# Performance work log

Measured on AMD Instinct MI355X. Metric: run time of the kernel, lower is better.

The kernel has to match this reference:

```python
import jax, jax.numpy as jnp
import numpy as np

N_NODES = 50000
N_EDGES = 800000
N_GRAPHS = 128
INPUT_DIM = 64
HIDDEN = 64       # num_heads * dim_per_head = 4 * 16
N_HEADS = 4
DK = HIDDEN // N_HEADS   # 16, per-head key/query dim
DV = HIDDEN // N_HEADS   # 16, per-head value dim
NUM_LAYERS = 4           # -> 3 GIN layers
OUT_DIM = 16
LN_EPS = 1e-5


def layer_norm(x, g, b):
    mu = jnp.mean(x, axis=-1, keepdims=True)
    var = jnp.mean(jnp.square(x - mu), axis=-1, keepdims=True)
    return (x - mu) * jax.lax.rsqrt(var + LN_EPS) * g + b


def sab_block(x, Wq, Wk, Wv, Wo, ln_g, ln_b, add_residual):
    # x: [N, S, D_in]; pre-LN self-attention block (Set Transformer SAB)
    xin = layer_norm(x, ln_g, ln_b)
    q = jnp.einsum('nsd,dhk->nshk', xin, Wq)   # [N,S,H,dk]
    k = jnp.einsum('nsd,dhk->nshk', xin, Wk)
    v = jnp.einsum('nsd,dhk->nshk', xin, Wv)   # [N,S,H,dv]
    scores = jnp.einsum('nqhk,nshk->nhqs', q, k) / jnp.sqrt(jnp.asarray(DK, x.dtype))
    att = jax.nn.softmax(scores, axis=-1)
    o = jnp.einsum('nhqs,nshk->nqhk', att, v)
    o = o.reshape(o.shape[0], o.shape[1], N_HEADS * DV)
    o = o @ Wo                                  # [N,S,dim_out]
    if add_residual:
        o = o + x
    return o


def gin_aggregate(h, src, dst):
    # sum-neighbor aggregation; eps=0, learn_eps=False -> (1+0)*h + sum_nbrs
    msg = jax.ops.segment_sum(h[src], dst, num_segments=N_NODES)
    return h + msg


def setup_inputs() -> dict:
    key = jax.random.key(0)
    ks = jax.random.split(key, 16)
    s = 0.05
    feat = jax.random.normal(ks[0], (N_NODES, 4 * INPUT_DIM), dtype=jnp.float32)
    src = jax.random.randint(ks[1], (N_EDGES,), 0, N_NODES)
    dst = jax.random.randint(ks[2], (N_EDGES,), 0, N_NODES)
    graph_ids = jnp.sort(jax.random.randint(ks[3], (N_NODES,), 0, N_GRAPHS))
    L = NUM_LAYERS - 1  # 3 GIN layers, all same shapes (input_dim == hidden)
    Wq = jax.random.normal(ks[4], (L, HIDDEN, N_HEADS, DK), dtype=jnp.float32) * s
    Wk = jax.random.normal(ks[5], (L, HIDDEN, N_HEADS, DK), dtype=jnp.float32) * s
    Wv = jax.random.normal(ks[6], (L, HIDDEN, N_HEADS, DV), dtype=jnp.float32) * s
    Wo = jax.random.normal(ks[7], (L, N_HEADS * DV, HIDDEN), dtype=jnp.float32) * s
    sab_ln_g = jnp.ones((L, HIDDEN), dtype=jnp.float32)
    sab_ln_b = jnp.zeros((L, HIDDEN), dtype=jnp.float32)
    ln1_g = jnp.ones((L, HIDDEN), dtype=jnp.float32)
    ln1_b = jnp.zeros((L, HIDDEN), dtype=jnp.float32)
    ln2_g = jnp.ones((L, HIDDEN), dtype=jnp.float32)
    ln2_b = jnp.zeros((L, HIDDEN), dtype=jnp.float32)
    W_pred = jax.random.normal(ks[8], (NUM_LAYERS, HIDDEN, OUT_DIM), dtype=jnp.float32) * s
    b_pred = jnp.zeros((NUM_LAYERS, OUT_DIM), dtype=jnp.float32)
    return {"feat": feat, "src": src, "dst": dst, "graph_ids": graph_ids,
            "Wq": Wq, "Wk": Wk, "Wv": Wv, "Wo": Wo,
            "sab_ln_g": sab_ln_g, "sab_ln_b": sab_ln_b,
            "ln1_g": ln1_g, "ln1_b": ln1_b, "ln2_g": ln2_g, "ln2_b": ln2_b,
            "W_pred": W_pred, "b_pred": b_pred}


def reference(feat, src, dst, graph_ids, Wq, Wk, Wv, Wo,
              sab_ln_g, sab_ln_b, ln1_g, ln1_b, ln2_g, ln2_b, W_pred, b_pred):
    h = feat.reshape(N_NODES, -1, INPUT_DIM)   # [N, S, D]
    hidden_rep = [h]
    for i in range(NUM_LAYERS - 1):
        if i == 0:
            agg = gin_aggregate(h, src, dst)
            h = sab_block(agg, Wq[i], Wk[i], Wv[i], Wo[i],
                          sab_ln_g[i], sab_ln_b[i], add_residual=False)
        else:
            h_pre = layer_norm(h, ln1_g[i], ln1_b[i])
            agg = gin_aggregate(h_pre, src, dst)
            h = h + sab_block(agg, Wq[i], Wk[i], Wv[i], Wo[i],
                              sab_ln_g[i], sab_ln_b[i], add_residual=True)
        hidden_rep.append(layer_norm(jax.nn.relu(h), ln2_g[i], ln2_b[i]))
    score = jnp.zeros((N_GRAPHS, hidden_rep[0].shape[1], OUT_DIM), dtype=feat.dtype)
    for i, hh in enumerate(hidden_rep):
        pooled = jax.ops.segment_sum(hh, graph_ids, num_segments=N_GRAPHS)  # [B,S,D]
        score = score + pooled @ W_pred[i] + b_pred[i]
    return score
```

## Files before the change

kernel.cpp:

```cpp
#include <hip/hip_runtime.h>

#define NN 50000
#define NE 800000
#define NG 128
#define RREP 16
#define RSTRIDE 50048

typedef __attribute__((ext_vector_type(8))) short short8;
typedef __attribute__((ext_vector_type(4))) float f32x4;

__device__ __forceinline__ unsigned short f2bf(float f){
  union { float f; unsigned int u; } v; v.f = f;
  return (unsigned short)((v.u + 0x7fffu + ((v.u >> 16) & 1u)) >> 16);
}
__device__ __forceinline__ float bf2f(unsigned short h){
  union { unsigned int u; float f; } v; v.u = ((unsigned int)h) << 16;
  return v.f;
}

__global__ __launch_bounds__(256) void k_goff(const int* __restrict__ gid,
                                              int* __restrict__ goff){
  int i = blockIdx.x*256 + threadIdx.x;
  if (i >= NN) return;
  int c = gid[i];
  int p = (i == 0) ? -1 : gid[i-1];
  for (int g = p+1; g <= c; ++g) goff[g] = i;
  if (i == NN-1){
    for (int g = c+1; g <= NG; ++g) goff[g] = NN;
  }
}

__global__ __launch_bounds__(256) void k_count_rep(const int* __restrict__ idx,
                                                   int* __restrict__ cnt_rep, int n){
  int i = blockIdx.x*256 + threadIdx.x;
  int r = blockIdx.x & (RREP-1);
  if (i < n) atomicAdd(&cnt_rep[r*RSTRIDE + idx[i]], 1);
}

__global__ __launch_bounds__(256) void k_reduce_rep(const int* __restrict__ cnt_rep,
                                                    int* __restrict__ cnt){
  int i = blockIdx.x*256 + threadIdx.x;
  if (i < NN){
    int s = 0;
    #pragma unroll
    for (int r=0; r<RREP; ++r) s += cnt_rep[r*RSTRIDE + i];
    cnt[i] = s;
  }
}

__global__ __launch_bounds__(256) void k_blocksum(const int* __restrict__ in, int n,
                                                  int* __restrict__ bsum){
  __shared__ int ws4[4];
  int i = blockIdx.x*256 + threadIdx.x;
  int v = (i < n) ? in[i] : 0;
  #pragma unroll
  for (int d=1; d<64; d<<=1) v += __shfl_xor(v, d);
  int lane = threadIdx.x & 63, w = threadIdx.x >> 6;
  if (lane == 0) ws4[w] = v;
  __syncthreads();
  if (threadIdx.x == 0) bsum[blockIdx.x] = ws4[0]+ws4[1]+ws4[2]+ws4[3];
}

__global__ __launch_bounds__(256) void k_scan_small(const int* __restrict__ in, int n,
                                                    int* __restrict__ out){
  __shared__ int wsum[4];
  int tid = threadIdx.x, lane = tid & 63, w = tid >> 6;
  int v = (tid < n) ? in[tid] : 0;
  int x = v;
  #pragma unroll
  for (int d=1; d<64; d<<=1){ int y = __shfl_up(x, d); if (lane >= d) x += y; }
  if (lane == 63) wsum[w] = x;
  __syncthreads();
  int pre2 = 0;
  for (int j=0; j<w; ++j) pre2 += wsum[j];
  int incl = x + pre2;
  if (tid < n) out[tid] = incl - v;
  if (tid == n-1) out[n] = incl;
}

__global__ __launch_bounds__(256) void k_scan_apply(const int* __restrict__ in, int n,
                                                    const int* __restrict__ boff,
                                                    int* __restrict__ out){
  __shared__ int wsum[4];
  int tid = threadIdx.x, lane = tid & 63, w = tid >> 6;
  int i = blockIdx.x*256 + tid;
  int v = (i < n) ? in[i] : 0;
  int x = v;
  #pragma unroll
  for (int d=1; d<64; d<<=1){ int y = __shfl_up(x, d); if (lane >= d) x += y; }
  if (lane == 63) wsum[w] = x;
  __syncthreads();
  int pre2 = boff[blockIdx.x];
  for (int j=0; j<w; ++j) pre2 += wsum[j];
  int excl = x - v + pre2;
  if (i < n){
    out[i] = excl;
    if (i == n-1) out[n] = excl + v;
  }
}

__global__ __launch_bounds__(256) void k_fpos_rep(const int* __restrict__ cnt_rep,
                                                  const int* __restrict__ off,
                                                  int* __restrict__ fpos_rep){
  int i = blockIdx.x*256 + threadIdx.x;
  if (i < NN){
    int p = off[i];
    #pragma unroll
    for (int r=0; r<RREP; ++r){
      fpos_rep[r*RSTRIDE + i] = p;
      p += cnt_rep[r*RSTRIDE + i];
    }
  }
}

__global__ __launch_bounds__(256) void k_fill_rep(const int* __restrict__ src,
                                                  const int* __restrict__ dst,
                                                  int* __restrict__ fpos_rep,
                                                  int* __restrict__ csr, int n){
  int i = blockIdx.x*256 + threadIdx.x;
  int r = blockIdx.x & (RREP-1);
  if (i < n){
    int p = atomicAdd(&fpos_rep[r*RSTRIDE + dst[i]], 1);
    csr[p] = src[i];
  }
}

__global__ __launch_bounds__(256) void k_wt(const float* __restrict__ Wq,
                                            const float* __restrict__ Wk,
                                            const float* __restrict__ Wv,
                                            const float* __restrict__ Wo,
                                            unsigned short* __restrict__ Wt){
  int gid = blockIdx.x*256 + threadIdx.x;
  int l   = gid >> 14;
  int rem = gid & 16383;
  int mat = rem >> 12;
  int idx = rem & 4095;
  int c = idx >> 6, n = idx & 63;
  const float* srcp = (mat==0)?Wq:(mat==1)?Wk:(mat==2)?Wv:Wo;
  float v = srcp[l*4096 + idx];
  Wt[l*16384 + (mat*64 + n)*64 + c] = f2bf(v);
}

__global__ __launch_bounds__(256) void k_f2bf(const float* __restrict__ in,
                                              unsigned short* __restrict__ out){
  int i = blockIdx.x*256 + threadIdx.x;
  float4 v = ((const float4*)in)[i];
  ushort4 o; o.x=f2bf(v.x); o.y=f2bf(v.y); o.z=f2bf(v.z); o.w=f2bf(v.w);
  ((ushort4*)out)[i] = o;
}

__global__ __launch_bounds__(256) void k_aggregate(const unsigned short* __restrict__ pre,
                                                   const int* __restrict__ off,
                                                   const int* __restrict__ csr,
                                                   float* __restrict__ agg){
  int w = threadIdx.x >> 6, lane = threadIdx.x & 63;
  int node = blockIdx.x*4 + w;
  int s = off[node], e = off[node+1];
  const ushort4* base = (const ushort4*)pre;
  ushort4 u = base[node*64 + lane];
  float a0 = bf2f(u.x), a1 = bf2f(u.y), a2 = bf2f(u.z), a3 = bf2f(u.w);
  int i = s;
  for (; i + 4 <= e; i += 4){
    int n0 = csr[i], n1 = csr[i+1], n2 = csr[i+2], n3 = csr[i+3];
    ushort4 u0 = base[n0*64 + lane], u1 = base[n1*64 + lane];
    ushort4 u2 = base[n2*64 + lane], u3 = base[n3*64 + lane];
    a0 += bf2f(u0.x)+bf2f(u1.x)+bf2f(u2.x)+bf2f(u3.x);
    a1 += bf2f(u0.y)+bf2f(u1.y)+bf2f(u2.y)+bf2f(u3.y);
    a2 += bf2f(u0.z)+bf2f(u1.z)+bf2f(u2.z)+bf2f(u3.z);
    a3 += bf2f(u0.w)+bf2f(u1.w)+bf2f(u2.w)+bf2f(u3.w);
  }
  for (; i < e; ++i){
    int n0 = csr[i];
    ushort4 u0 = base[n0*64 + lane];
    a0 += bf2f(u0.x); a1 += bf2f(u0.y); a2 += bf2f(u0.z); a3 += bf2f(u0.w);
  }
  ((float4*)agg)[node*64 + lane] = make_float4(a0, a1, a2, a3);
}

__global__ __launch_bounds__(256) void k_sab(float* __restrict__ agg,
                                             float* __restrict__ h,
                                             unsigned short* __restrict__ pre_next,
                                             const unsigned short* __restrict__ Wt,
                                             const float* __restrict__ lng,
                                             const float* __restrict__ lnb,
                                             const float* __restrict__ g2,
                                             const float* __restrict__ b2,
                                             const float* __restrict__ g1,
                                             const float* __restrict__ b1,
                                             int residual, int write_pre){
  __shared__ unsigned short xo_s[4][16][72];
  __shared__ unsigned short qkv_s[4][16][200];

  int tid = threadIdx.x;
  int w = tid >> 6, lane = tid & 63;
  int c16 = lane & 15, kb = lane >> 4;
  int R0 = blockIdx.x*64 + w*16;

  {
    float4 gv = ((const float4*)lng)[c16];
    float4 bv = ((const float4*)lnb)[c16];
    #pragma unroll
    for (int rr=0; rr<4; ++rr){
      int m = rr*4 + kb;
      float4 v = ((const float4*)agg)[(R0+m)*16 + c16];
      float s = v.x+v.y+v.z+v.w;
      float q = v.x*v.x+v.y*v.y+v.z*v.z+v.w*v.w;
      #pragma unroll
      for (int d=1; d<16; d<<=1){ s += __shfl_xor(s, d); q += __shfl_xor(q, d); }
      float mu = s*(1.f/64.f);
      float rs = rsqrtf(q*(1.f/64.f) - mu*mu + 1e-5f);
      ushort4 o;
      o.x=f2bf((v.x-mu)*rs*gv.x+bv.x); o.y=f2bf((v.y-mu)*rs*gv.y+bv.y);
      o.z=f2bf((v.z-mu)*rs*gv.z+bv.z); o.w=f2bf((v.w-mu)*rs*gv.w+bv.w);
      *(ushort4*)&xo_s[w][m][c16*4] = o;
    }
  }

  short8 a0 = *(const short8*)&xo_s[w][c16][kb*8];
  short8 a1 = *(const short8*)&xo_s[w][c16][32 + kb*8];
  f32x4 acc[12];
  #pragma unroll
  for (int t=0; t<12; ++t){
    short8 b0 = *(const short8*)&Wt[(t*16 + c16)*64 + kb*8];
    short8 b1 = *(const short8*)&Wt[(t*16 + c16)*64 + 32 + kb*8];
    f32x4 z = {0.f, 0.f, 0.f, 0.f};
    z = __builtin_amdgcn_mfma_f32_16x16x32_bf16(a0, b0, z, 0, 0, 0);
    z = __builtin_amdgcn_mfma_f32_16x16x32_bf16(a1, b1, z, 0, 0, 0);
    acc[t] = z;
  }
  #pragma unroll
  for (int t=0; t<12; ++t){
    #pragma unroll
    for (int r=0; r<4; ++r)
      qkv_s[w][kb*4 + r][t*16 + c16] = f2bf(acc[t][r]);
  }

  {
    int p = lane >> 2, qr = lane & 3;
    int ns = p >> 2, hd = p & 3;
    int mrow = ns*4 + qr;
    int qc = hd*16, kc = 64 + hd*16, vc = 128 + hd*16;
    float qv[16];
    short8 u0 = *(const short8*)&qkv_s[w][mrow][qc];
    short8 u1 = *(const short8*)&qkv_s[w][mrow][qc+8];
    #pragma unroll
    for (int j=0; j<8; ++j){
      qv[j]   = bf2f((unsigned short)u0[j]);
      qv[8+j] = bf2f((unsigned short)u1[j]);
    }
    float sc[4];
    #pragma unroll
    for (int kr=0; kr<4; ++kr){
      short8 k0 = *(const short8*)&qkv_s[w][ns*4+kr][kc];
      short8 k1 = *(const short8*)&qkv_s[w][ns*4+kr][kc+8];
      float d2 = 0.f;
      #pragma unroll
      for (int j=0; j<8; ++j){
        d2 += qv[j]  *bf2f((unsigned short)k0[j]);
        d2 += qv[8+j]*bf2f((unsigned short)k1[j]);
      }
      sc[kr] = d2 * 0.25f;
    }
    float mx = fmaxf(fmaxf(sc[0],sc[1]), fmaxf(sc[2],sc[3]));
    float e0=__expf(sc[0]-mx), e1=__expf(sc[1]-mx), e2=__expf(sc[2]-mx), e3=__expf(sc[3]-mx);
    float inv = 1.f/(e0+e1+e2+e3);
    float at[4] = {e0*inv, e1*inv, e2*inv, e3*inv};
    float ov[16];
    #pragma unroll
    for (int j=0; j<16; ++j) ov[j] = 0.f;
    #pragma unroll
    for (int kr=0; kr<4; ++kr){
      short8 v0 = *(const short8*)&qkv_s[w][ns*4+kr][vc];
      short8 v1 = *(const short8*)&qkv_s[w][ns*4+kr][vc+8];
      #pragma unroll
      for (int j=0; j<8; ++j){
        ov[j]   += at[kr]*bf2f((unsigned short)v0[j]);
        ov[8+j] += at[kr]*bf2f((unsigned short)v1[j]);
      }
    }
    short8 s0v, s1v;
    #pragma unroll
    for (int j=0; j<8; ++j){
      s0v[j] = (short)f2bf(ov[j]);
      s1v[j] = (short)f2bf(ov[8+j]);
    }
    *(short8*)&xo_s[w][mrow][qc]   = s0v;
    *(short8*)&xo_s[w][mrow][qc+8] = s1v;
  }

  short8 oa0 = *(const short8*)&xo_s[w][c16][kb*8];
  short8 oa1 = *(const short8*)&xo_s[w][c16][32 + kb*8];
  float val[4][4];
  #pragma unroll
  for (int t=0; t<4; ++t){
    short8 b0 = *(const short8*)&Wt[(192 + t*16 + c16)*64 + kb*8];
    short8 b1 = *(const short8*)&Wt[(192 + t*16 + c16)*64 + 32 + kb*8];
    f32x4 z = {0.f, 0.f, 0.f, 0.f};
    z = __builtin_amdgcn_mfma_f32_16x16x32_bf16(oa0, b0, z, 0, 0, 0);
    z = __builtin_amdgcn_mfma_f32_16x16x32_bf16(oa1, b1, z, 0, 0, 0);
    #pragma unroll
    for (int r=0; r<4; ++r){
      float v = z[r];
      if (residual){
        int gi = (R0 + kb*4 + r)*64 + t*16 + c16;
        v += h[gi] + agg[gi];
      }
      val[t][r] = v;
    }
  }

  float s1[4], q1[4], s2[4], q2[4];
  #pragma unroll
  for (int r=0; r<4; ++r){
    float a=0.f, b=0.f, c=0.f, d=0.f;
    #pragma unroll
    for (int t=0; t<4; ++t){
      float v = val[t][r];
      float rv = fmaxf(v, 0.f);
      a += v; b += v*v; c += rv; d += rv*rv;
    }
    s1[r]=a; q1[r]=b; s2[r]=c; q2[r]=d;
  }
  #pragma unroll
  for (int d=1; d<16; d<<=1){
    #pragma unroll
    for (int r=0; r<4; ++r){
      s1[r] += __shfl_xor(s1[r], d); q1[r] += __shfl_xor(q1[r], d);
      s2[r] += __shfl_xor(s2[r], d); q2[r] += __shfl_xor(q2[r], d);
    }
  }
  float mu1[4], rs1[4], mu2[4], rs2[4];
  #pragma unroll
  for (int r=0; r<4; ++r){
    mu1[r] = s1[r]*(1.f/64.f);
    rs1[r] = rsqrtf(q1[r]*(1.f/64.f) - mu1[r]*mu1[r] + 1e-5f);
    mu2[r] = s2[r]*(1.f/64.f);
    rs2[r] = rsqrtf(q2[r]*(1.f/64.f) - mu2[r]*mu2[r] + 1e-5f);
  }
  #pragma unroll
  for (int t=0; t<4; ++t){
    int col = t*16 + c16;
    float g2v = g2[col], b2v = b2[col];
    float g1v = 0.f, b1v = 0.f;
    if (write_pre){ g1v = g1[col]; b1v = b1[col]; }
    #pragma unroll
    for (int r=0; r<4; ++r){
      int gi = (R0 + kb*4 + r)*64 + col;
      float v = val[t][r];
      h[gi] = v;
      float rv = fmaxf(v, 0.f);
      agg[gi] = (rv - mu2[r])*rs2[r]*g2v + b2v;
      if (write_pre)
        pre_next[gi] = f2bf((v - mu1[r])*rs1[r]*g1v + b1v);
    }
  }
}

__global__ __launch_bounds__(256) void k_pool8(const float* __restrict__ src,
                                               const int* __restrict__ goff,
                                               float* __restrict__ out){
  int g = blockIdx.x >> 3, sub = blockIdx.x & 7, t = threadIdx.x;
  int s = goff[g], e = goff[g+1], len = e - s;
  int s0 = s + ((len*sub) >> 3), e0 = s + ((len*(sub+1)) >> 3);
  float a0=0.f, a1=0.f;
  int n = s0;
  for (; n + 2 <= e0; n += 2){ a0 += src[n*256 + t]; a1 += src[(n+1)*256 + t]; }
  if (n < e0) a0 += src[n*256 + t];
  atomicAdd(&out[g*256 + t], a0 + a1);
}

__global__ __launch_bounds__(256) void k_final(const float* __restrict__ pooled,
                                               const float* __restrict__ Wp,
                                               const float* __restrict__ bp,
                                               float* __restrict__ out){
  int t = blockIdx.x*256 + threadIdx.x;
  int b = t >> 6, s = (t >> 4) & 3, o = t & 15;
  float acc = 0.f;
  for (int i=0; i<4; ++i){
    acc += bp[i*16 + o];
    const float* pr = pooled + i*32768 + b*256 + s*64;
    const float* wp = Wp + i*1024 + o;
    float a = 0.f;
    #pragma unroll 8
    for (int c=0; c<64; ++c) a += pr[c]*wp[c*16];
    acc += a;
  }
  out[t] = acc;
}

static const size_t OFF_H    = 0;
static const size_t OFF_AGG  = 51200000;
static const size_t OFF_PRE  = 102400000;
static const size_t OFF_CSR  = 128000000;
static const size_t OFF_CNT  = 131200000;
static const size_t OFF_OFF  = 131400064;
static const size_t OFF_GOFF = 131800768;
static const size_t OFF_POOL = 131801920;
static const size_t OFF_WT   = 132326208;
static const size_t OFF_BSUM = 132424576;
static const size_t OFF_BOFF = 132425472;

extern "C" void kernel_launch(void* const* d_in, const int* in_sizes, int n_in,
                              void* d_out, int out_size, void* d_ws, size_t ws_size,
                              hipStream_t stream) {
  const float* feat = (const float*)d_in[0];
  const int*   src  = (const int*)d_in[1];
  const int*   dst  = (const int*)d_in[2];
  const int*   gid  = (const int*)d_in[3];
  const float* Wq   = (const float*)d_in[4];
  const float* Wk   = (const float*)d_in[5];
  const float* Wv   = (const float*)d_in[6];
  const float* Wo   = (const float*)d_in[7];
  const float* sg   = (const float*)d_in[8];
  const float* sb   = (const float*)d_in[9];
  const float* l1g  = (const float*)d_in[10];
  const float* l1b  = (const float*)d_in[11];
  const float* l2g  = (const float*)d_in[12];
  const float* l2b  = (const float*)d_in[13];
  const float* Wp   = (const float*)d_in[14];
  const float* bp   = (const float*)d_in[15];
  float* out = (float*)d_out;

  char* ws = (char*)d_ws;
  float*          h      = (float*)(ws + OFF_H);
  float*          agg    = (float*)(ws + OFF_AGG);
  unsigned short* pre    = (unsigned short*)(ws + OFF_PRE);
  int*            csr    = (int*)(ws + OFF_CSR);
  int*            cnt    = (int*)(ws + OFF_CNT);
  int*            off    = (int*)(ws + OFF_OFF);
  int*            goff   = (int*)(ws + OFF_GOFF);
  float*          pooled = (float*)(ws + OFF_POOL);
  unsigned short* Wt     = (unsigned short*)(ws + OFF_WT);
  int*            bsum   = (int*)(ws + OFF_BSUM);
  int*            boff   = (int*)(ws + OFF_BOFF);
  int*            cnt_rep  = (int*)(ws + OFF_H);
  int*            fpos_rep = (int*)(ws + OFF_H + (size_t)RREP*RSTRIDE*4);

  hipMemsetAsync(cnt_rep, 0, (size_t)RREP*RSTRIDE*4, stream);
  hipMemsetAsync(pooled, 0, 4*NG*256*sizeof(float), stream);

  k_count_rep<<<NE/256, 256, 0, stream>>>(dst, cnt_rep, NE);
  k_goff<<<(NN+255)/256, 256, 0, stream>>>(gid, goff);
  k_reduce_rep<<<(NN+255)/256, 256, 0, stream>>>(cnt_rep, cnt);
  k_blocksum<<<196, 256, 0, stream>>>(cnt, NN, bsum);
  k_scan_small<<<1, 256, 0, stream>>>(bsum, 196, boff);
  k_scan_apply<<<196, 256, 0, stream>>>(cnt, NN, boff, off);
  k_fpos_rep<<<(NN+255)/256, 256, 0, stream>>>(cnt_rep, off, fpos_rep);
  k_fill_rep<<<NE/256, 256, 0, stream>>>(src, dst, fpos_rep, csr, NE);

  k_wt<<<192, 256, 0, stream>>>(Wq, Wk, Wv, Wo, Wt);
  k_f2bf<<<12500, 256, 0, stream>>>(feat, pre);
  k_pool8<<<NG*8, 256, 0, stream>>>(feat, goff, pooled + 0*32768);

  k_aggregate<<<12500, 256, 0, stream>>>(pre, off, csr, agg);
  k_sab<<<3125, 256, 0, stream>>>(agg, h, pre, Wt + 0*16384,
                                  sg + 0, sb + 0, l2g + 0, l2b + 0,
                                  l1g + 1*64, l1b + 1*64, 0, 1);
  k_pool8<<<NG*8, 256, 0, stream>>>(agg, goff, pooled + 1*32768);

  for (int i = 1; i < 3; ++i){
    k_aggregate<<<12500, 256, 0, stream>>>(pre, off, csr, agg);
    int wp = (i < 2) ? 1 : 0;
    k_sab<<<3125, 256, 0, stream>>>(agg, h, pre, Wt + i*16384,
                                    sg + i*64, sb + i*64, l2g + i*64, l2b + i*64,
                                    l1g + (i+1)*64, l1b + (i+1)*64, 1, wp);
    k_pool8<<<NG*8, 256, 0, stream>>>(agg, goff, pooled + (i+1)*32768);
  }

  k_final<<<32, 256, 0, stream>>>(pooled, Wp, bp, out);
}
```

Measured before the change: 698.9 us.

## Store aggregate and hidden activations in bf16 and skip last h write

```diff
diff --git a/kernel.cpp b/kernel.cpp
--- a/kernel.cpp
+++ b/kernel.cpp
@@ -152,7 +152,7 @@
 __global__ __launch_bounds__(256) void k_aggregate(const unsigned short* __restrict__ pre,
                                                    const int* __restrict__ off,
                                                    const int* __restrict__ csr,
-                                                   float* __restrict__ agg){
+                                                   unsigned short* __restrict__ agg){
   int w = threadIdx.x >> 6, lane = threadIdx.x & 63;
   int node = blockIdx.x*4 + w;
   int s = off[node], e = off[node+1];
@@ -174,11 +174,12 @@
     ushort4 u0 = base[n0*64 + lane];
     a0 += bf2f(u0.x); a1 += bf2f(u0.y); a2 += bf2f(u0.z); a3 += bf2f(u0.w);
   }
-  ((float4*)agg)[node*64 + lane] = make_float4(a0, a1, a2, a3);
-}
-
-__global__ __launch_bounds__(256) void k_sab(float* __restrict__ agg,
-                                             float* __restrict__ h,
+  ushort4 o; o.x=f2bf(a0); o.y=f2bf(a1); o.z=f2bf(a2); o.w=f2bf(a3);
+  ((ushort4*)agg)[node*64 + lane] = o;
+}
+
+__global__ __launch_bounds__(256) void k_sab(unsigned short* __restrict__ agg,
+                                             unsigned short* __restrict__ h,
                                              unsigned short* __restrict__ pre_next,
                                              const unsigned short* __restrict__ Wt,
                                              const float* __restrict__ lng,
@@ -187,7 +188,7 @@
                                              const float* __restrict__ b2,
                                              const float* __restrict__ g1,
                                              const float* __restrict__ b1,
-                                             int residual, int write_pre){
+                                             int residual, int write_pre, int write_h){
   __shared__ unsigned short xo_s[4][16][72];
   __shared__ unsigned short qkv_s[4][16][200];
 
@@ -202,16 +203,17 @@
     #pragma unroll
     for (int rr=0; rr<4; ++rr){
       int m = rr*4 + kb;
-      float4 v = ((const float4*)agg)[(R0+m)*16 + c16];
-      float s = v.x+v.y+v.z+v.w;
-      float q = v.x*v.x+v.y*v.y+v.z*v.z+v.w*v.w;
+      ushort4 uv = ((const ushort4*)agg)[(R0+m)*16 + c16];
+      float vx = bf2f(uv.x), vy = bf2f(uv.y), vz = bf2f(uv.z), vw = bf2f(uv.w);
+      float s = vx+vy+vz+vw;
+      float q = vx*vx+vy*vy+vz*vz+vw*vw;
       #pragma unroll
       for (int d=1; d<16; d<<=1){ s += __shfl_xor(s, d); q += __shfl_xor(q, d); }
       float mu = s*(1.f/64.f);
       float rs = rsqrtf(q*(1.f/64.f) - mu*mu + 1e-5f);
       ushort4 o;
-      o.x=f2bf((v.x-mu)*rs*gv.x+bv.x); o.y=f2bf((v.y-mu)*rs*gv.y+bv.y);
-      o.z=f2bf((v.z-mu)*rs*gv.z+bv.z); o.w=f2bf((v.w-mu)*rs*gv.w+bv.w);
+      o.x=f2bf((vx-mu)*rs*gv.x+bv.x); o.y=f2bf((vy-mu)*rs*gv.y+bv.y);
+      o.z=f2bf((vz-mu)*rs*gv.z+bv.z); o.w=f2bf((vw-mu)*rs*gv.w+bv.w);
       *(ushort4*)&xo_s[w][m][c16*4] = o;
     }
   }
@@ -303,7 +305,7 @@
       float v = z[r];
       if (residual){
         int gi = (R0 + kb*4 + r)*64 + t*16 + c16;
-        v += h[gi] + agg[gi];
+        v += bf2f(h[gi]) + bf2f(agg[gi]);
       }
       val[t][r] = v;
     }
@@ -347,9 +349,9 @@
     for (int r=0; r<4; ++r){
       int gi = (R0 + kb*4 + r)*64 + col;
       float v = val[t][r];
-      h[gi] = v;
+      if (write_h) h[gi] = f2bf(v);
       float rv = fmaxf(v, 0.f);
-      agg[gi] = (rv - mu2[r])*rs2[r]*g2v + b2v;
+      agg[gi] = f2bf((rv - mu2[r])*rs2[r]*g2v + b2v);
       if (write_pre)
         pre_next[gi] = f2bf((v - mu1[r])*rs1[r]*g1v + b1v);
     }
@@ -366,6 +368,19 @@
   int n = s0;
   for (; n + 2 <= e0; n += 2){ a0 += src[n*256 + t]; a1 += src[(n+1)*256 + t]; }
   if (n < e0) a0 += src[n*256 + t];
+  atomicAdd(&out[g*256 + t], a0 + a1);
+}
+
+__global__ __launch_bounds__(256) void k_pool8b(const unsigned short* __restrict__ src,
+                                                const int* __restrict__ goff,
+                                                float* __restrict__ out){
+  int g = blockIdx.x >> 3, sub = blockIdx.x & 7, t = threadIdx.x;
+  int s = goff[g], e = goff[g+1], len = e - s;
+  int s0 = s + ((len*sub) >> 3), e0 = s + ((len*(sub+1)) >> 3);
+  float a0=0.f, a1=0.f;
+  int n = s0;
+  for (; n + 2 <= e0; n += 2){ a0 += bf2f(src[n*256 + t]); a1 += bf2f(src[(n+1)*256 + t]); }
+  if (n < e0) a0 += bf2f(src[n*256 + t]);
   atomicAdd(&out[g*256 + t], a0 + a1);
 }
 
@@ -389,16 +404,16 @@
 }
 
 static const size_t OFF_H    = 0;
-static const size_t OFF_AGG  = 51200000;
-static const size_t OFF_PRE  = 102400000;
-static const size_t OFF_CSR  = 128000000;
-static const size_t OFF_CNT  = 131200000;
-static const size_t OFF_OFF  = 131400064;
-static const size_t OFF_GOFF = 131800768;
-static const size_t OFF_POOL = 131801920;
-static const size_t OFF_WT   = 132326208;
-static const size_t OFF_BSUM = 132424576;
-static const size_t OFF_BOFF = 132425472;
+static const size_t OFF_AGG  = 25600000;
+static const size_t OFF_PRE  = 51200000;
+static const size_t OFF_CSR  = 76800000;
+static const size_t OFF_CNT  = 80000000;
+static const size_t OFF_OFF  = 80200064;
+static const size_t OFF_GOFF = 80400128;
+static const size_t OFF_POOL = 80400704;
+static const size_t OFF_WT   = 80924992;
+static const size_t OFF_BSUM = 81023296;
+static const size_t OFF_BOFF = 81024128;
 
 extern "C" void kernel_launch(void* const* d_in, const int* in_sizes, int n_in,
                               void* d_out, int out_size, void* d_ws, size_t ws_size,
@@ -422,8 +437,8 @@
   float* out = (float*)d_out;
 
   char* ws = (char*)d_ws;
-  float*          h      = (float*)(ws + OFF_H);
-  float*          agg    = (float*)(ws + OFF_AGG);
+  unsigned short* h      = (unsigned short*)(ws + OFF_H);
+  unsigned short* agg    = (unsigned short*)(ws + OFF_AGG);
   unsigned short* pre    = (unsigned short*)(ws + OFF_PRE);
   int*            csr    = (int*)(ws + OFF_CSR);
   int*            cnt    = (int*)(ws + OFF_CNT);
@@ -455,16 +470,17 @@
   k_aggregate<<<12500, 256, 0, stream>>>(pre, off, csr, agg);
   k_sab<<<3125, 256, 0, stream>>>(agg, h, pre, Wt + 0*16384,
                                   sg + 0, sb + 0, l2g + 0, l2b + 0,
-                                  l1g + 1*64, l1b + 1*64, 0, 1);
-  k_pool8<<<NG*8, 256, 0, stream>>>(agg, goff, pooled + 1*32768);
+                                  l1g + 1*64, l1b + 1*64, 0, 1, 1);
+  k_pool8b<<<NG*8, 256, 0, stream>>>(agg, goff, pooled + 1*32768);
 
   for (int i = 1; i < 3; ++i){
     k_aggregate<<<12500, 256, 0, stream>>>(pre, off, csr, agg);
     int wp = (i < 2) ? 1 : 0;
+    int wh = (i < 2) ? 1 : 0;
     k_sab<<<3125, 256, 0, stream>>>(agg, h, pre, Wt + i*16384,
                                     sg + i*64, sb + i*64, l2g + i*64, l2b + i*64,
-                                    l1g + (i+1)*64, l1b + (i+1)*64, 1, wp);
-    k_pool8<<<NG*8, 256, 0, stream>>>(agg, goff, pooled + (i+1)*32768);
+                                    l1g + (i+1)*64, l1b + (i+1)*64, 1, wp, wh);
+    k_pool8b<<<NG*8, 256, 0, stream>>>(agg, goff, pooled + (i+1)*32768);
   }
 
   k_final<<<32, 256, 0, stream>>>(pooled, Wp, bp, out);
```

New measurement: 670.4 us. 4.1% less time.
